# Kernel optimization log

Measured on AMD Instinct MI355X. Metric: run time of the kernel, lower is better.

Reference implementation:

```python
import jax, jax.numpy as jnp
import numpy as np

N, E = 50000, 800000
CUR, HID, OUT = 128, 96, 128
NEG_SLOPE = 0.01  # F.leaky_relu default


def setup_inputs() -> dict:
    key = jax.random.key(0)
    ks = jax.random.split(key, 12)
    inv = lambda d: 1.0 / np.sqrt(d)
    return {
        "h": jax.random.normal(ks[0], (N, CUR), jnp.float32),
        "x": jax.random.normal(ks[1], (N, CUR), jnp.float32),
        "edge_index": jax.random.randint(ks[2], (2, E), 0, N, dtype=jnp.int64),
        "edge_weight": jax.random.uniform(ks[3], (E,), jnp.float32),
        # preprocessor_x: Linear(cur_dim, hidden_dim)
        "pre_W": jax.random.uniform(ks[4], (CUR, HID), jnp.float32, -inv(CUR), inv(CUR)),
        "pre_b": jax.random.uniform(ks[5], (HID,), jnp.float32, -inv(CUR), inv(CUR)),
        # SAGEConv(hidden, out): lin_l (neighbor, with bias) + lin_r (root, no bias)
        "sage_Wl": jax.random.uniform(ks[6], (HID, OUT), jnp.float32, -inv(HID), inv(HID)),
        "sage_bl": jnp.zeros((OUT,), jnp.float32),
        "sage_Wr": jax.random.uniform(ks[7], (HID, OUT), jnp.float32, -inv(HID), inv(HID)),
        # ARMAConv(hidden, out) with K=1 stacks, T=1 layers (PyG defaults)
        "arma_W": jax.random.uniform(ks[8], (HID, OUT), jnp.float32, -inv(HID), inv(HID)),
        "arma_V": jax.random.uniform(ks[9], (HID, OUT), jnp.float32, -inv(HID), inv(HID)),
        "arma_b": jnp.zeros((OUT,), jnp.float32),
    }


def _cell(x, src, dst, edge_weight, pre_W, pre_b,
          sage_Wl, sage_bl, sage_Wr, arma_W, arma_V, arma_b):
    n = x.shape[0]
    xh = x @ pre_W + pre_b  # [N, HID]

    # ---- SAGEConv: mean aggregation of edge-weighted neighbor features ----
    msg = xh[src] * edge_weight[:, None]                     # [E, HID]
    aggr = jax.ops.segment_sum(msg, dst, num_segments=n)     # [N, HID]
    cnt = jax.ops.segment_sum(jnp.ones_like(edge_weight), dst, num_segments=n)
    mean = aggr / jnp.maximum(cnt, 1.0)[:, None]
    o_sage = mean @ sage_Wl + sage_bl + xh @ sage_Wr         # [N, OUT]

    # ---- ARMAConv (K=1, T=1): ReLU(L_hat (x W) + x V + b) ----
    deg = jax.ops.segment_sum(edge_weight, dst, num_segments=n)
    dinv = jnp.where(deg > 0, jax.lax.rsqrt(jnp.maximum(deg, 1e-30)), 0.0)
    norm = dinv[src] * edge_weight * dinv[dst]               # [E]
    xw = xh @ arma_W                                         # [N, OUT]
    prop = jax.ops.segment_sum(xw[src] * norm[:, None], dst, num_segments=n)
    o_arma = jax.nn.relu(prop + xh @ arma_V + arma_b)        # [N, OUT]

    o1 = jax.nn.leaky_relu(o_sage, NEG_SLOPE)
    o2 = jax.nn.leaky_relu(o_arma, NEG_SLOPE)
    return jax.nn.relu(o1 + o2)


def reference(h, x, edge_index, edge_weight, pre_W, pre_b,
              sage_Wl, sage_bl, sage_Wr, arma_W, arma_V, arma_b):
    src, dst = edge_index[0], edge_index[1]
    his = x
    o3 = _cell(x, src, dst, edge_weight, pre_W, pre_b,
               sage_Wl, sage_bl, sage_Wr, arma_W, arma_V, arma_b)
    return (his, o3)
```

## Files before the change

### kernel.cpp

```cpp
#include <hip/hip_runtime.h>


typedef __attribute__((ext_vector_type(8))) short bf16x8;
typedef __attribute__((ext_vector_type(4))) float f32x4;

__device__ __forceinline__ float bf2f(unsigned short u) {
    return __uint_as_float(((unsigned)u) << 16);
}
__device__ __forceinline__ unsigned short f2bf(float f) {
    unsigned u = __float_as_uint(f);
    return (unsigned short)((u + 0x7FFFu + ((u >> 16) & 1u)) >> 16);
}

__device__ __forceinline__ int edge_src(const int* ei, int e, int E, int flag) {
    return flag ? ei[2 * e] : ei[e];
}
__device__ __forceinline__ int edge_dst(const int* ei, int e, int E, int flag) {
    return flag ? ei[2 * (E + e)] : ei[E + e];
}

__global__ void k_wprep(const unsigned* __restrict__ eiu,
                        const float* __restrict__ Wl, const float* __restrict__ Wr,
                        const float* __restrict__ Wa, const float* __restrict__ Va,
                        const float* __restrict__ preW,
                        unsigned short* __restrict__ Wf_s,
                        unsigned short* __restrict__ Wf_a,
                        unsigned short* __restrict__ Wfp,
                        int* __restrict__ flag,
                        int4* __restrict__ cnt4, int nz4) {
    if (blockIdx.x == 0) {
        __shared__ int bad;
        if (threadIdx.x == 0) bad = 0;
        __syncthreads();
        int nb = 0;
#pragma unroll
        for (int q = 0; q < 4; q++) {
            unsigned w = eiu[2 * (threadIdx.x * 4 + q) + 1];
            if (w != 0) nb++;
        }
        if (nb) atomicAdd(&bad, nb);
        __syncthreads();
        if (threadIdx.x == 0) *flag = (bad == 0) ? 1 : 0;
        return;
    }
    int tid = (blockIdx.x - 1) * blockDim.x + threadIdx.x;
    if (tid < 6144) {
        int mat = tid / 3072, rem = tid % 3072;
        int kstep = rem / 512, rem2 = rem % 512;
        int g = rem2 / 128, j = rem2 % 128;
        int k0 = kstep * 32 + g * 8;
        const float* Wtop = mat ? Wa : Wl;
        const float* Wbot = mat ? Va : Wr;
        unsigned short* dst = (mat ? Wf_a : Wf_s) + (((size_t)(kstep * 4 + g) * 128 + j) * 8);
#pragma unroll
        for (int kk = 0; kk < 8; kk++) {
            int k = k0 + kk;
            float v = (k < 96) ? Wtop[k * 128 + j] : Wbot[(k - 96) * 128 + j];
            dst[kk] = f2bf(v);
        }
    } else if (tid < 7680) {
        int rem = tid - 6144;
        int kstep = rem / 384, rem2 = rem % 384;
        int g = rem2 / 96, j = rem2 % 96;
        int k0 = kstep * 32 + g * 8;
        unsigned short* dst = Wfp + (((size_t)(kstep * 4 + g) * 96 + j) * 8);
#pragma unroll
        for (int kk = 0; kk < 8; kk++) dst[kk] = f2bf(preW[(k0 + kk) * 96 + j]);
    } else if (tid >= 8192 && tid < 8192 + nz4) {
        cnt4[tid - 8192] = make_int4(0, 0, 0, 0);
    }
}

__global__ __launch_bounds__(256) void k_xh_count(
    const float* __restrict__ x, const unsigned short* __restrict__ Wfp,
    const float* __restrict__ b, unsigned short* __restrict__ xhbf,
    float* __restrict__ out0, int N, int xhBlocks,
    const int* __restrict__ ei, int* __restrict__ cntS, int* __restrict__ pos,
    int E, const int* __restrict__ flagp) {
    __shared__ unsigned short X[64][136];
    if (blockIdx.x >= xhBlocks) {
        int e = (blockIdx.x - xhBlocks) * 256 + threadIdx.x;
        if (e < E) {
            int flag = *flagp;
            int d = edge_dst(ei, e, E, flag);
            int shard = blockIdx.x & 7;
            int lp = atomicAdd(&cntS[(size_t)shard * N + d], 1);
            pos[e] = (lp << 3) | shard;
        }
        return;
    }
    int t = threadIdx.x;
    int nb = blockIdx.x * 64;
    for (int u = t; u < 2048; u += 256) {
        int row = u >> 5, q = u & 31;
        long gn = nb + row;
        float4 v = make_float4(0.f, 0.f, 0.f, 0.f);
        if (gn < N) {
            v = ((const float4*)(x + gn * 128))[q];
            ((float4*)(out0 + gn * 128))[q] = v;
        }
        unsigned short* p = &X[row][q * 4];
        p[0] = f2bf(v.x); p[1] = f2bf(v.y); p[2] = f2bf(v.z); p[3] = f2bf(v.w);
    }
    __syncthreads();
    int lane = t & 63, w = t >> 6;
    int lr = lane & 15, lg = lane >> 4;
    bf16x8 a[4];
#pragma unroll
    for (int ks = 0; ks < 4; ks++)
        a[ks] = *(const bf16x8*)&X[w * 16 + lr][ks * 32 + lg * 8];
    for (int jt = 0; jt < 6; jt++) {
        f32x4 acc = {0.f, 0.f, 0.f, 0.f};
#pragma unroll
        for (int ks = 0; ks < 4; ks++) {
            bf16x8 bf = *(const bf16x8*)(Wfp + (((size_t)(ks * 4 + lg) * 96 + jt * 16 + lr) * 8));
            acc = __builtin_amdgcn_mfma_f32_16x16x32_bf16(a[ks], bf, acc, 0, 0, 0);
        }
        int h = jt * 16 + lr;
        float bb = b[h];
#pragma unroll
        for (int r = 0; r < 4; r++) {
            long n = nb + w * 16 + lg * 4 + r;
            if (n < N) xhbf[n * 96 + h] = f2bf(acc[r] + bb);
        }
    }
}

__global__ void k_scan_blk(const int* __restrict__ cntS, int* __restrict__ sdelta,
                           int* __restrict__ offs, int* __restrict__ bsum, int N) {
    __shared__ int sh[256];
    int t = threadIdx.x;
    int n = blockIdx.x * 256 + t;
    int total = 0;
    if (n < N) {
        int run = 0;
#pragma unroll
        for (int s = 0; s < 8; s++) {
            sdelta[(size_t)s * N + n] = run;
            run += cntS[(size_t)s * N + n];
        }
        total = run;
    }
    sh[t] = total;
    __syncthreads();
    for (int off = 1; off < 256; off <<= 1) {
        int add = (t >= off) ? sh[t - off] : 0;
        __syncthreads();
        sh[t] += add;
        __syncthreads();
    }
    if (n < N) offs[n + 1] = sh[t];
    if (t == 255) bsum[blockIdx.x] = sh[255];
    if (blockIdx.x == 0 && t == 0) offs[0] = 0;
}

__global__ void k_scan_add(int* __restrict__ offs, const int* __restrict__ bsum, int N) {
    __shared__ int sh[256];
    int t = threadIdx.x;
    sh[t] = (t < (int)blockIdx.x) ? bsum[t] : 0;
    __syncthreads();
    for (int s = 128; s > 0; s >>= 1) {
        if (t < s) sh[t] += sh[t + s];
        __syncthreads();
    }
    int base = sh[0];
    int n = blockIdx.x * 256 + t;
    if (n < N && blockIdx.x > 0) offs[n + 1] += base;
}

__global__ void k_fill(const int* __restrict__ ei, const float* __restrict__ ew,
                       const int* __restrict__ offs, const int* __restrict__ sdelta,
                       const int* __restrict__ pos, int* __restrict__ esrc,
                       float* __restrict__ eww, int E, int N,
                       const int* __restrict__ flagp) {
    int e = blockIdx.x * blockDim.x + threadIdx.x;
    if (e >= E) return;
    int flag = *flagp;
    int s = edge_src(ei, e, E, flag);
    int d = edge_dst(ei, e, E, flag);
    int pp = pos[e];
    int shard = pp & 7, lp = pp >> 3;
    int idx = offs[d] + sdelta[(size_t)shard * N + d] + lp;
    esrc[idx] = s;
    eww[idx] = ew[e];
}

__global__ void k_degcsr(const float* __restrict__ eww, const int* __restrict__ offs,
                         float* __restrict__ dinv, float* __restrict__ minv, int N) {
    int n = blockIdx.x * blockDim.x + threadIdx.x;
    if (n >= N) return;
    int beg = offs[n], end = offs[n + 1];
    float dg = 0.f;
    for (int e = beg; e < end; e++) dg += eww[e];
    dinv[n] = dg > 0.f ? rsqrtf(fmaxf(dg, 1e-30f)) : 0.f;
    minv[n] = 1.f / fmaxf((float)(end - beg), 1.f);
}

__global__ __launch_bounds__(256) void k_gather(
    const int* __restrict__ esrc, const float* __restrict__ eww,
    const unsigned short* __restrict__ xhbf, const int* __restrict__ offs,
    const float* __restrict__ dinv, const float* __restrict__ minv,
    unsigned short* __restrict__ meanbf, unsigned short* __restrict__ propbf, int N) {
    int lane = threadIdx.x & 63;
    int d = __builtin_amdgcn_readfirstlane(blockIdx.x * 4 + (threadIdx.x >> 6));
    if (d >= N) return;
    int beg = offs[d], end = offs[d + 1];
    bool act = lane < 48;
    int col = 2 * lane;
    float s0 = 0.f, s1 = 0.f, a0 = 0.f, a1 = 0.f;
    int e = beg;
    for (; e + 8 <= end; e += 8) {
        int idx[8]; float wgt[8], dv[8]; unsigned v[8];
#pragma unroll
        for (int q = 0; q < 8; q++) { idx[q] = esrc[e + q]; wgt[q] = eww[e + q]; }
#pragma unroll
        for (int q = 0; q < 8; q++) dv[q] = dinv[idx[q]];
#pragma unroll
        for (int q = 0; q < 8; q++)
            v[q] = act ? *(const unsigned*)(xhbf + (size_t)idx[q] * 96 + col) : 0u;
#pragma unroll
        for (int q = 0; q < 8; q++) {
            float x0 = bf2f((unsigned short)(v[q] & 0xffff));
            float x1 = bf2f((unsigned short)(v[q] >> 16));
            float w2 = wgt[q], dw = dv[q] * w2;
            s0 += w2 * x0; s1 += w2 * x1;
            a0 += dw * x0; a1 += dw * x1;
        }
    }
    for (; e + 4 <= end; e += 4) {
        int idx[4]; float wgt[4], dv[4]; unsigned v[4];
#pragma unroll
        for (int q = 0; q < 4; q++) { idx[q] = esrc[e + q]; wgt[q] = eww[e + q]; }
#pragma unroll
        for (int q = 0; q < 4; q++) dv[q] = dinv[idx[q]];
#pragma unroll
        for (int q = 0; q < 4; q++)
            v[q] = act ? *(const unsigned*)(xhbf + (size_t)idx[q] * 96 + col) : 0u;
#pragma unroll
        for (int q = 0; q < 4; q++) {
            float x0 = bf2f((unsigned short)(v[q] & 0xffff));
            float x1 = bf2f((unsigned short)(v[q] >> 16));
            float w2 = wgt[q], dw = dv[q] * w2;
            s0 += w2 * x0; s1 += w2 * x1;
            a0 += dw * x0; a1 += dw * x1;
        }
    }
    for (; e < end; e++) {
        int s = esrc[e];
        float w2 = eww[e];
        float ds = dinv[s];
        if (act) {
            unsigned v = *(const unsigned*)(xhbf + (size_t)s * 96 + col);
            float x0 = bf2f((unsigned short)(v & 0xffff));
            float x1 = bf2f((unsigned short)(v >> 16));
            s0 += w2 * x0; s1 += w2 * x1;
            a0 += ds * w2 * x0; a1 += ds * w2 * x1;
        }
    }
    if (act) {
        float mi = minv[d], di = dinv[d];
        unsigned mo = (unsigned)f2bf(s0 * mi) | ((unsigned)f2bf(s1 * mi) << 16);
        unsigned po = (unsigned)f2bf(a0 * di) | ((unsigned)f2bf(a1 * di) << 16);
        *(unsigned*)(meanbf + (size_t)d * 96 + col) = mo;
        *(unsigned*)(propbf + (size_t)d * 96 + col) = po;
    }
}

__global__ __launch_bounds__(256) void k_out(
    const unsigned short* __restrict__ meanbf, const unsigned short* __restrict__ propbf,
    const unsigned short* __restrict__ xhbf, const unsigned short* __restrict__ Wf_s,
    const unsigned short* __restrict__ Wf_a, const float* __restrict__ bl,
    const float* __restrict__ ba, float* __restrict__ out, int N) {
    __shared__ unsigned short A[3][64][104];
    int t = threadIdx.x;
    int nb = blockIdx.x * 64;
    for (int u = t; u < 2304; u += 256) {
        int arr = u / 768, rem = u - arr * 768;
        int row = rem / 12, c = rem - row * 12;
        long gn = nb + row;
        const unsigned short* src = (arr == 0) ? meanbf : (arr == 1) ? propbf : xhbf;
        float4 v = (gn < N) ? *(const float4*)(src + gn * 96 + c * 8)
                            : make_float4(0.f, 0.f, 0.f, 0.f);
        *(float4*)&A[arr][row][c * 8] = v;
    }
    __syncthreads();
    int lane = t & 63, w = t >> 6;
    int lr = lane & 15, lg = lane >> 4;
    bf16x8 am[3], ap[3], ax[3];
#pragma unroll
    for (int ks = 0; ks < 3; ks++) {
        int row = w * 16 + lr, kc = ks * 32 + lg * 8;
        am[ks] = *(const bf16x8*)&A[0][row][kc];
        ap[ks] = *(const bf16x8*)&A[1][row][kc];
        ax[ks] = *(const bf16x8*)&A[2][row][kc];
    }
    for (int jt = 0; jt < 8; jt++) {
        f32x4 accS = {0.f, 0.f, 0.f, 0.f};
        f32x4 accA = {0.f, 0.f, 0.f, 0.f};
#pragma unroll
        for (int ks = 0; ks < 3; ks++) {
            size_t boffS = ((size_t)(ks * 4 + lg) * 128 + jt * 16 + lr) * 8;
            size_t boffS2 = ((size_t)((ks + 3) * 4 + lg) * 128 + jt * 16 + lr) * 8;
            bf16x8 b0 = *(const bf16x8*)(Wf_s + boffS);
            bf16x8 b1 = *(const bf16x8*)(Wf_s + boffS2);
            bf16x8 b2 = *(const bf16x8*)(Wf_a + boffS);
            bf16x8 b3 = *(const bf16x8*)(Wf_a + boffS2);
            accS = __builtin_amdgcn_mfma_f32_16x16x32_bf16(am[ks], b0, accS, 0, 0, 0);
            accS = __builtin_amdgcn_mfma_f32_16x16x32_bf16(ax[ks], b1, accS, 0, 0, 0);
            accA = __builtin_amdgcn_mfma_f32_16x16x32_bf16(ap[ks], b2, accA, 0, 0, 0);
            accA = __builtin_amdgcn_mfma_f32_16x16x32_bf16(ax[ks], b3, accA, 0, 0, 0);
        }
        int j = jt * 16 + lr;
        float blj = bl[j], baj = ba[j];
#pragma unroll
        for (int r = 0; r < 4; r++) {
            long n = nb + w * 16 + lg * 4 + r;
            if (n < N) {
                float os = accS[r] + blj;
                float oa = fmaxf(accA[r] + baj, 0.f);
                float o1 = os > 0.f ? os : 0.01f * os;
                float o2 = oa > 0.f ? oa : 0.01f * oa;
                out[n * 128 + j] = fmaxf(o1 + o2, 0.f);
            }
        }
    }
}

extern "C" void kernel_launch(void* const* d_in, const int* in_sizes, int n_in,
                              void* d_out, int out_size, void* d_ws, size_t ws_size,
                              hipStream_t stream) {
    const float* x    = (const float*)d_in[1];
    const int*   ei   = (const int*)d_in[2];
    const float* ew   = (const float*)d_in[3];
    const float* preW = (const float*)d_in[4];
    const float* preb = (const float*)d_in[5];
    const float* Wl   = (const float*)d_in[6];
    const float* bl   = (const float*)d_in[7];
    const float* Wr   = (const float*)d_in[8];
    const float* Wa   = (const float*)d_in[9];
    const float* Va   = (const float*)d_in[10];
    const float* ba   = (const float*)d_in[11];

    const int N = in_sizes[1] / 128;
    const int E = in_sizes[3];
    const int NB = (N + 255) / 256;

    char* w = (char*)d_ws;
    unsigned short* xhbf   = (unsigned short*)w; w += (size_t)N * 96 * 2;
    unsigned short* meanbf = (unsigned short*)w; w += (size_t)N * 96 * 2;
    unsigned short* propbf = (unsigned short*)w; w += (size_t)N * 96 * 2;
    unsigned short* Wf_s   = (unsigned short*)w; w += (size_t)6 * 4 * 128 * 8 * 2;
    unsigned short* Wf_a   = (unsigned short*)w; w += (size_t)6 * 4 * 128 * 8 * 2;
    unsigned short* Wfp    = (unsigned short*)w; w += (size_t)4 * 4 * 96 * 8 * 2;
    int*   esrc   = (int*)w;   w += (size_t)E * 4;
    float* eww    = (float*)w; w += (size_t)E * 4;
    int*   pos    = (int*)w;   w += (size_t)E * 4;
    int*   cntS   = (int*)w;   w += (size_t)8 * N * 4;
    int*   sdelta = (int*)w;   w += (size_t)8 * N * 4;
    float* dinv   = (float*)w; w += (size_t)N * 4;
    float* minv   = (float*)w; w += (size_t)N * 4;
    int*   offs   = (int*)w;   w += (size_t)(N + 1) * 4;
    int*   bsum   = (int*)w;   w += 256 * 4;
    int*   flag   = (int*)w;

    const int nz4 = (8 * N + 3) / 4;
    const int wprep_blocks = 1 + (8192 + nz4 + 255) / 256;
    const int xhBlocks = (N + 63) / 64;
    const int cntBlocks = (E + 255) / 256;

    k_wprep<<<wprep_blocks, 256, 0, stream>>>((const unsigned*)ei, Wl, Wr, Wa, Va,
                                              preW, Wf_s, Wf_a, Wfp, flag,
                                              (int4*)cntS, nz4);
    k_xh_count<<<xhBlocks + cntBlocks, 256, 0, stream>>>(
        x, Wfp, preb, xhbf, (float*)d_out, N, xhBlocks, ei, cntS, pos, E, flag);
    k_scan_blk<<<NB, 256, 0, stream>>>(cntS, sdelta, offs, bsum, N);
    k_scan_add<<<NB, 256, 0, stream>>>(offs, bsum, N);
    k_fill<<<(E + 255) / 256, 256, 0, stream>>>(ei, ew, offs, sdelta, pos, esrc,
                                                eww, E, N, flag);
    k_degcsr<<<NB, 256, 0, stream>>>(eww, offs, dinv, minv, N);
    k_gather<<<(N + 3) / 4, 256, 0, stream>>>(esrc, eww, xhbf, offs, dinv,
                                              minv, meanbf, propbf, N);
    k_out<<<(N + 63) / 64, 256, 0, stream>>>(meanbf, propbf, xhbf, Wf_s, Wf_a,
                                             bl, ba, (float*)d_out + (size_t)N * 128, N);
}
```

Measured before the change: 146.5 us.

## Fuse neighbor gather into output GEMM kernel via shared memory

Merges the CSR gather kernel and the MFMA output kernel into one 512-thread kernel. Each block aggregates mean and propagated features for its 64 nodes directly into LDS and then runs the GEMM from LDS, split across 8 waves by row group and column half. This removes the global write and re-read of the two bf16 intermediate arrays and one kernel launch. In exchange each wave handles 8 nodes serially, which may lower gather parallelism and latency hiding, and rows with many edges can unbalance a block.

```diff
diff --git a/kernel.cpp b/kernel.cpp
--- a/kernel.cpp
+++ b/kernel.cpp
@@ -196,105 +196,102 @@
     minv[n] = 1.f / fmaxf((float)(end - beg), 1.f);
 }
 
-__global__ __launch_bounds__(256) void k_gather(
+__global__ __launch_bounds__(512) void k_go(
     const int* __restrict__ esrc, const float* __restrict__ eww,
     const unsigned short* __restrict__ xhbf, const int* __restrict__ offs,
     const float* __restrict__ dinv, const float* __restrict__ minv,
-    unsigned short* __restrict__ meanbf, unsigned short* __restrict__ propbf, int N) {
-    int lane = threadIdx.x & 63;
-    int d = __builtin_amdgcn_readfirstlane(blockIdx.x * 4 + (threadIdx.x >> 6));
-    if (d >= N) return;
-    int beg = offs[d], end = offs[d + 1];
-    bool act = lane < 48;
-    int col = 2 * lane;
-    float s0 = 0.f, s1 = 0.f, a0 = 0.f, a1 = 0.f;
-    int e = beg;
-    for (; e + 8 <= end; e += 8) {
-        int idx[8]; float wgt[8], dv[8]; unsigned v[8];
-#pragma unroll
-        for (int q = 0; q < 8; q++) { idx[q] = esrc[e + q]; wgt[q] = eww[e + q]; }
-#pragma unroll
-        for (int q = 0; q < 8; q++) dv[q] = dinv[idx[q]];
-#pragma unroll
-        for (int q = 0; q < 8; q++)
-            v[q] = act ? *(const unsigned*)(xhbf + (size_t)idx[q] * 96 + col) : 0u;
-#pragma unroll
-        for (int q = 0; q < 8; q++) {
-            float x0 = bf2f((unsigned short)(v[q] & 0xffff));
-            float x1 = bf2f((unsigned short)(v[q] >> 16));
-            float w2 = wgt[q], dw = dv[q] * w2;
-            s0 += w2 * x0; s1 += w2 * x1;
-            a0 += dw * x0; a1 += dw * x1;
-        }
-    }
-    for (; e + 4 <= end; e += 4) {
-        int idx[4]; float wgt[4], dv[4]; unsigned v[4];
-#pragma unroll
-        for (int q = 0; q < 4; q++) { idx[q] = esrc[e + q]; wgt[q] = eww[e + q]; }
-#pragma unroll
-        for (int q = 0; q < 4; q++) dv[q] = dinv[idx[q]];
-#pragma unroll
-        for (int q = 0; q < 4; q++)
-            v[q] = act ? *(const unsigned*)(xhbf + (size_t)idx[q] * 96 + col) : 0u;
-#pragma unroll
-        for (int q = 0; q < 4; q++) {
-            float x0 = bf2f((unsigned short)(v[q] & 0xffff));
-            float x1 = bf2f((unsigned short)(v[q] >> 16));
-            float w2 = wgt[q], dw = dv[q] * w2;
-            s0 += w2 * x0; s1 += w2 * x1;
-            a0 += dw * x0; a1 += dw * x1;
-        }
-    }
-    for (; e < end; e++) {
-        int s = esrc[e];
-        float w2 = eww[e];
-        float ds = dinv[s];
-        if (act) {
-            unsigned v = *(const unsigned*)(xhbf + (size_t)s * 96 + col);
-            float x0 = bf2f((unsigned short)(v & 0xffff));
-            float x1 = bf2f((unsigned short)(v >> 16));
-            s0 += w2 * x0; s1 += w2 * x1;
-            a0 += ds * w2 * x0; a1 += ds * w2 * x1;
-        }
-    }
-    if (act) {
-        float mi = minv[d], di = dinv[d];
-        unsigned mo = (unsigned)f2bf(s0 * mi) | ((unsigned)f2bf(s1 * mi) << 16);
-        unsigned po = (unsigned)f2bf(a0 * di) | ((unsigned)f2bf(a1 * di) << 16);
-        *(unsigned*)(meanbf + (size_t)d * 96 + col) = mo;
-        *(unsigned*)(propbf + (size_t)d * 96 + col) = po;
-    }
-}
-
-__global__ __launch_bounds__(256) void k_out(
-    const unsigned short* __restrict__ meanbf, const unsigned short* __restrict__ propbf,
-    const unsigned short* __restrict__ xhbf, const unsigned short* __restrict__ Wf_s,
-    const unsigned short* __restrict__ Wf_a, const float* __restrict__ bl,
-    const float* __restrict__ ba, float* __restrict__ out, int N) {
+    const unsigned short* __restrict__ Wf_s, const unsigned short* __restrict__ Wf_a,
+    const float* __restrict__ bl, const float* __restrict__ ba,
+    float* __restrict__ out, int N) {
     __shared__ unsigned short A[3][64][104];
     int t = threadIdx.x;
     int nb = blockIdx.x * 64;
-    for (int u = t; u < 2304; u += 256) {
-        int arr = u / 768, rem = u - arr * 768;
-        int row = rem / 12, c = rem - row * 12;
+    int wv = t >> 6, lane = t & 63;
+    for (int u = t; u < 768; u += 512) {
+        int row = u / 12, c = u - row * 12;
         long gn = nb + row;
-        const unsigned short* src = (arr == 0) ? meanbf : (arr == 1) ? propbf : xhbf;
-        float4 v = (gn < N) ? *(const float4*)(src + gn * 96 + c * 8)
+        float4 v = (gn < N) ? *(const float4*)(xhbf + gn * 96 + c * 8)
                             : make_float4(0.f, 0.f, 0.f, 0.f);
-        *(float4*)&A[arr][row][c * 8] = v;
+        *(float4*)&A[2][row][c * 8] = v;
+    }
+    bool act = lane < 48;
+    int col = 2 * lane;
+    for (int i = 0; i < 8; i++) {
+        int row = wv * 8 + i;
+        int d = nb + row;
+        if (d >= N) break;
+        int beg = offs[d], end = offs[d + 1];
+        float s0 = 0.f, s1 = 0.f, a0 = 0.f, a1 = 0.f;
+        int e = beg;
+        for (; e + 8 <= end; e += 8) {
+            int idx[8]; float wgt[8], dv[8]; unsigned v[8];
+#pragma unroll
+            for (int q = 0; q < 8; q++) { idx[q] = esrc[e + q]; wgt[q] = eww[e + q]; }
+#pragma unroll
+            for (int q = 0; q < 8; q++) dv[q] = dinv[idx[q]];
+#pragma unroll
+            for (int q = 0; q < 8; q++)
+                v[q] = act ? *(const unsigned*)(xhbf + (size_t)idx[q] * 96 + col) : 0u;
+#pragma unroll
+            for (int q = 0; q < 8; q++) {
+                float x0 = bf2f((unsigned short)(v[q] & 0xffff));
+                float x1 = bf2f((unsigned short)(v[q] >> 16));
+                float w2 = wgt[q], dw = dv[q] * w2;
+                s0 += w2 * x0; s1 += w2 * x1;
+                a0 += dw * x0; a1 += dw * x1;
+            }
+        }
+        for (; e + 4 <= end; e += 4) {
+            int idx[4]; float wgt[4], dv[4]; unsigned v[4];
+#pragma unroll
+            for (int q = 0; q < 4; q++) { idx[q] = esrc[e + q]; wgt[q] = eww[e + q]; }
+#pragma unroll
+            for (int q = 0; q < 4; q++) dv[q] = dinv[idx[q]];
+#pragma unroll
+            for (int q = 0; q < 4; q++)
+                v[q] = act ? *(const unsigned*)(xhbf + (size_t)idx[q] * 96 + col) : 0u;
+#pragma unroll
+            for (int q = 0; q < 4; q++) {
+                float x0 = bf2f((unsigned short)(v[q] & 0xffff));
+                float x1 = bf2f((unsigned short)(v[q] >> 16));
+                float w2 = wgt[q], dw = dv[q] * w2;
+                s0 += w2 * x0; s1 += w2 * x1;
+                a0 += dw * x0; a1 += dw * x1;
+            }
+        }
+        for (; e < end; e++) {
+            int s = esrc[e];
+            float w2 = eww[e];
+            float ds = dinv[s];
+            if (act) {
+                unsigned v = *(const unsigned*)(xhbf + (size_t)s * 96 + col);
+                float x0 = bf2f((unsigned short)(v & 0xffff));
+                float x1 = bf2f((unsigned short)(v >> 16));
+                s0 += w2 * x0; s1 += w2 * x1;
+                a0 += ds * w2 * x0; a1 += ds * w2 * x1;
+            }
+        }
+        if (act) {
+            float mi = minv[d], di = dinv[d];
+            unsigned mo = (unsigned)f2bf(s0 * mi) | ((unsigned)f2bf(s1 * mi) << 16);
+            unsigned po = (unsigned)f2bf(a0 * di) | ((unsigned)f2bf(a1 * di) << 16);
+            *(unsigned*)&A[0][row][col] = mo;
+            *(unsigned*)&A[1][row][col] = po;
+        }
     }
     __syncthreads();
-    int lane = t & 63, w = t >> 6;
+    int rg = wv & 3, jh = wv >> 2;
     int lr = lane & 15, lg = lane >> 4;
     bf16x8 am[3], ap[3], ax[3];
 #pragma unroll
     for (int ks = 0; ks < 3; ks++) {
-        int row = w * 16 + lr, kc = ks * 32 + lg * 8;
+        int row = rg * 16 + lr, kc = ks * 32 + lg * 8;
         am[ks] = *(const bf16x8*)&A[0][row][kc];
         ap[ks] = *(const bf16x8*)&A[1][row][kc];
         ax[ks] = *(const bf16x8*)&A[2][row][kc];
     }
-    for (int jt = 0; jt < 8; jt++) {
+    for (int jq = 0; jq < 4; jq++) {
+        int jt = jh * 4 + jq;
         f32x4 accS = {0.f, 0.f, 0.f, 0.f};
         f32x4 accA = {0.f, 0.f, 0.f, 0.f};
 #pragma unroll
@@ -314,7 +311,7 @@
         float blj = bl[j], baj = ba[j];
 #pragma unroll
         for (int r = 0; r < 4; r++) {
-            long n = nb + w * 16 + lg * 4 + r;
+            long n = nb + rg * 16 + lg * 4 + r;
             if (n < N) {
                 float os = accS[r] + blj;
                 float oa = fmaxf(accA[r] + baj, 0.f);
@@ -347,8 +344,6 @@
 
     char* w = (char*)d_ws;
     unsigned short* xhbf   = (unsigned short*)w; w += (size_t)N * 96 * 2;
-    unsigned short* meanbf = (unsigned short*)w; w += (size_t)N * 96 * 2;
-    unsigned short* propbf = (unsigned short*)w; w += (size_t)N * 96 * 2;
     unsigned short* Wf_s   = (unsigned short*)w; w += (size_t)6 * 4 * 128 * 8 * 2;
     unsigned short* Wf_a   = (unsigned short*)w; w += (size_t)6 * 4 * 128 * 8 * 2;
     unsigned short* Wfp    = (unsigned short*)w; w += (size_t)4 * 4 * 96 * 8 * 2;
@@ -378,8 +373,7 @@
     k_fill<<<(E + 255) / 256, 256, 0, stream>>>(ei, ew, offs, sdelta, pos, esrc,
                                                 eww, E, N, flag);
     k_degcsr<<<NB, 256, 0, stream>>>(eww, offs, dinv, minv, N);
-    k_gather<<<(N + 3) / 4, 256, 0, stream>>>(esrc, eww, xhbf, offs, dinv,
-                                              minv, meanbf, propbf, N);
-    k_out<<<(N + 63) / 64, 256, 0, stream>>>(meanbf, propbf, xhbf, Wf_s, Wf_a,
-                                             bl, ba, (float*)d_out + (size_t)N * 128, N);
-}
+    k_go<<<(N + 63) / 64, 512, 0, stream>>>(esrc, eww, xhbf, offs, dinv, minv,
+                                            Wf_s, Wf_a, bl, ba,
+                                            (float*)d_out + (size_t)N * 128, N);
+}
```

Result: slower. 169.2 us (+15.5%).
